# Kernel optimization log

Hardware: AMD Instinct MI355X
Metric: run time of the kernel (lower is better)

## Reference

```python
import jax, jax.numpy as jnp
import numpy as np

S = 3072       # packed sequence length
DIM = 1280     # hidden dim
H = 16         # num heads
HD = DIM // H  # head dim = 80
NEG = -1e9     # additive mask value for cross-segment entries


def setup_inputs() -> dict:
    key = jax.random.key(0)
    ks = jax.random.split(key, 6)
    x = jax.random.normal(ks[0], (S, DIM), jnp.float32)
    # rope angle table [S, HD//2]
    rotary_pos_emb = jax.random.uniform(ks[1], (S, HD // 2), jnp.float32, 0.0, 2.0 * np.pi)
    # 4 equal image segments packed together
    cu_seqlens = jnp.array([0, 768, 1536, 2304, 3072], jnp.int32)
    w_qkv = jax.random.normal(ks[2], (3 * DIM, DIM), jnp.float32) * 0.02
    b_qkv = jax.random.normal(ks[3], (3 * DIM,), jnp.float32) * 0.02
    w_proj = jax.random.normal(ks[4], (DIM, DIM), jnp.float32) * 0.02
    b_proj = jax.random.normal(ks[5], (DIM,), jnp.float32) * 0.02
    return {"x": x, "cu_seqlens": cu_seqlens, "rotary_pos_emb": rotary_pos_emb,
            "w_qkv": w_qkv, "b_qkv": b_qkv, "w_proj": w_proj, "b_proj": b_proj}


def _rope(t, cos, sin):
    # t: [S, H, HD]; cos/sin: [S, 1, HD]
    t1, t2 = jnp.split(t, 2, axis=-1)
    rot = jnp.concatenate([-t2, t1], axis=-1)
    return t * cos + rot * sin


def reference(x, cu_seqlens, rotary_pos_emb, w_qkv, b_qkv, w_proj, b_proj):
    s, d = x.shape
    qkv = (x @ w_qkv.T + b_qkv).reshape(s, 3, H, HD)
    q, k, v = qkv[:, 0], qkv[:, 1], qkv[:, 2]  # each [S, H, HD]

    # NeoX-style rope with tiled (repeated) freqs, computed in fp32
    cos = jnp.cos(rotary_pos_emb)
    sin = jnp.sin(rotary_pos_emb)
    cos = jnp.concatenate([cos, cos], axis=-1)[:, None, :]  # [S,1,HD]
    sin = jnp.concatenate([sin, sin], axis=-1)[:, None, :]
    q = _rope(q.astype(jnp.float32), cos, sin).astype(x.dtype)
    k = _rope(k.astype(jnp.float32), cos, sin).astype(x.dtype)

    # block-diagonal varlen mask from cu_seqlens: segment id per position
    seg = jnp.searchsorted(cu_seqlens, jnp.arange(s), side='right') - 1  # [S]
    mask = jnp.where(seg[:, None] == seg[None, :], 0.0, NEG).astype(x.dtype)  # [S,S]

    scale = 1.0 / np.sqrt(HD).astype(np.float32)
    scores = jnp.einsum('qhd,khd->hqk', q, k) * scale + mask[None]  # [H,S,S]
    attn = jax.nn.softmax(scores, axis=-1)
    out = jnp.einsum('hqk,khd->qhd', attn, v).reshape(s, d)  # [S, DIM]
    return out @ w_proj.T + b_proj
```

## Files before the change

### kernel.cpp

```cpp
#include <hip/hip_runtime.h>


typedef __bf16 bf16;
typedef __bf16 bf16x4 __attribute__((ext_vector_type(4)));
typedef __bf16 bf16x8 __attribute__((ext_vector_type(8)));
typedef float f32x4 __attribute__((ext_vector_type(4)));
typedef float f32x16 __attribute__((ext_vector_type(16)));
typedef unsigned int u32;

constexpr int S = 3072;
constexpr int DIM = 1280;
constexpr int H = 16;
constexpr int HD = 80;
constexpr int KDP = 128;
constexpr int NQKV = 3 * DIM;

constexpr int MB_A = S / 256;
constexpr int NB_B = NQKV / 256;
constexpr int NKT = DIM / 32;

constexpr float QSCALE = 1.4426950408889634f / 8.94427190999916f;

__device__ __forceinline__ void gload_lds16(const void* g, void* l) {
  __builtin_amdgcn_global_load_lds(
      (const __attribute__((address_space(1))) void*)g,
      (__attribute__((address_space(3))) void*)l, 16, 0, 0);
}

__device__ __forceinline__ u32 pkbf2(float a, float b) {
  union { bf16 h[2]; u32 w; } u;
  u.h[0] = (bf16)a; u.h[1] = (bf16)b;
  return u.w;
}

constexpr long PA_CHUNKS = (long)MB_A * NKT * 1024;
constexpr long PB_CHUNKS = (long)NB_B * NKT * 1024;
constexpr long PW_CHUNKS = (long)DIM * DIM / 8;

__global__ __launch_bounds__(256) void pack_inputs(
    const float* __restrict__ x, const float* __restrict__ wq,
    const float* __restrict__ wp, bf16* __restrict__ pA,
    bf16* __restrict__ pB, bf16* __restrict__ wp16) {
  long t = (long)blockIdx.x * 256 + threadIdx.x;
  const float* src;
  bf16* dst;
  if (t < PA_CHUNKS + PB_CHUNKS) {
    int blk, rem;
    const float* base;
    bf16* obase;
    if (t < PA_CHUNKS) {
      blk = (int)(t / (NKT * 1024)); rem = (int)(t % (NKT * 1024));
      base = x; obase = pA + t * 8;
    } else {
      long t2 = t - PA_CHUNKS;
      blk = (int)(t2 / (NKT * 1024)); rem = (int)(t2 % (NKT * 1024));
      base = wq; obase = pB + t2 * 8;
    }
    const int kt = rem >> 10, c = rem & 1023;
    const int lin = c * 16;
    const int logi = lin ^ (((lin >> 7) & 7) << 4);
    const int row = logi >> 6, col = (logi & 63) >> 1;
    src = base + (size_t)(blk * 256 + row) * DIM + kt * 32 + col;
    dst = obase;
  } else {
    long t2 = t - PA_CHUNKS - PB_CHUNKS;
    src = wp + t2 * 8;
    dst = wp16 + t2 * 8;
  }
  float4 v0 = *(const float4*)src;
  float4 v1 = *(const float4*)(src + 4);
  bf16x8 o = {(bf16)v0.x, (bf16)v0.y, (bf16)v0.z, (bf16)v0.w,
              (bf16)v1.x, (bf16)v1.y, (bf16)v1.z, (bf16)v1.w};
  *(bf16x8*)dst = o;
}

template <bool OUT_BF16>
__global__ __launch_bounds__(512, 2) void gemm256(
    const bf16* __restrict__ pA, const bf16* __restrict__ pB,
    const float* __restrict__ bias, void* __restrict__ Cout, int M, int N,
    int K) {
  extern __shared__ char lds[];
  const int tid = threadIdx.x;
  const int w = tid >> 6, lane = tid & 63;
  const int r15 = lane & 15, b4 = lane >> 4;
  const int wr = w >> 2, wc = w & 3;
  const int nwg = gridDim.x * gridDim.y;
  const int orig = blockIdx.y * gridDim.x + blockIdx.x;
  const int xcd = orig % 8, loc = orig / 8;
  const int qq = nwg / 8, rq = nwg % 8;
  const int swzid =
      (xcd < rq ? xcd * (qq + 1) : rq * (qq + 1) + (xcd - rq) * qq) + loc;
  const int nb = swzid % gridDim.x, mb = swzid / gridDim.x;
  const int n0 = nb * 256, m0 = mb * 256;
  const char* aPanel = (const char*)pA + (size_t)mb * NKT * 16384;
  const char* bPanel = (const char*)pB + (size_t)nb * NKT * 16384;
  const int NT = K / 32;
  auto stageA = [&](int kt) {
    char* s = lds + (kt & 3) * 32768;
    const char* g = aPanel + (size_t)kt * 16384;
    gload_lds16(g + tid * 16, s + tid * 16);
    gload_lds16(g + 8192 + tid * 16, s + 8192 + tid * 16);
  };
  auto stageB = [&](int kt) {
    char* s = lds + (kt & 3) * 32768 + 16384;
    const char* g = bPanel + (size_t)kt * 16384;
    gload_lds16(g + tid * 16, s + tid * 16);
    gload_lds16(g + 8192 + tid * 16, s + 8192 + tid * 16);
  };
  f32x4 acc[8][4] = {};
  stageA(0); stageB(0); stageA(1); stageB(1); stageA(2); stageB(2);
  asm volatile("s_waitcnt vmcnt(8)" ::: "memory");
  __builtin_amdgcn_s_barrier();
  for (int kt = 0; kt < NT; ++kt) {
    const char* As = lds + (kt & 3) * 32768;
    const char* Bs = As + 16384;
    const bool pf = (kt + 3 < NT);
    bf16x8 afr[4], bfr[4];
#pragma unroll
    for (int i = 0; i < 4; i++) {
      int a = (wr * 128 + i * 16 + r15) * 64 + b4 * 16;
      a ^= ((a >> 7) & 7) << 4;
      afr[i] = *(const bf16x8*)(As + a);
    }
#pragma unroll
    for (int j = 0; j < 4; j++) {
      int a = (wc * 64 + j * 16 + r15) * 64 + b4 * 16;
      a ^= ((a >> 7) & 7) << 4;
      bfr[j] = *(const bf16x8*)(Bs + a);
    }
    if (pf) stageA(kt + 3);
    asm volatile("" ::: "memory");
    __builtin_amdgcn_s_barrier();
    __builtin_amdgcn_s_setprio(1);
#pragma unroll
    for (int i = 0; i < 4; i++)
#pragma unroll
      for (int j = 0; j < 4; j++)
        acc[i][j] = __builtin_amdgcn_mfma_f32_16x16x32_bf16(afr[i], bfr[j],
                                                            acc[i][j], 0, 0, 0);
    __builtin_amdgcn_s_setprio(0);
    asm volatile("" ::: "memory");
    __builtin_amdgcn_s_barrier();
#pragma unroll
    for (int i = 0; i < 4; i++) {
      int a = (wr * 128 + 64 + i * 16 + r15) * 64 + b4 * 16;
      a ^= ((a >> 7) & 7) << 4;
      afr[i] = *(const bf16x8*)(As + a);
    }
    if (pf) stageB(kt + 3);
    asm volatile("" ::: "memory");
    __builtin_amdgcn_s_barrier();
    __builtin_amdgcn_s_setprio(1);
#pragma unroll
    for (int i = 0; i < 4; i++)
#pragma unroll
      for (int j = 0; j < 4; j++)
        acc[4 + i][j] = __builtin_amdgcn_mfma_f32_16x16x32_bf16(
            afr[i], bfr[j], acc[4 + i][j], 0, 0, 0);
    __builtin_amdgcn_s_setprio(0);
    const int rem = NT - 2 - kt;
    if (rem >= 2)      asm volatile("s_waitcnt vmcnt(8)" ::: "memory");
    else if (rem == 1) asm volatile("s_waitcnt vmcnt(4)" ::: "memory");
    else if (rem == 0) asm volatile("s_waitcnt vmcnt(0)" ::: "memory");
    else               asm volatile("" ::: "memory");
    __builtin_amdgcn_s_barrier();
  }
#pragma unroll
  for (int j = 0; j < 4; j++) {
    const int n = n0 + wc * 64 + j * 16 + r15;
    const float bv = bias[n];
#pragma unroll
    for (int i = 0; i < 8; i++) {
      const int mr = m0 + wr * 128 + i * 16 + b4 * 4;
#pragma unroll
      for (int r = 0; r < 4; r++) {
        float v = acc[i][j][r] + bv;
        if (OUT_BF16)
          ((bf16*)Cout)[(size_t)(mr + r) * N + n] = (bf16)v;
        else
          ((float*)Cout)[(size_t)(mr + r) * N + n] = v;
      }
    }
  }
}

template <bool OUT_BF16>
__global__ __launch_bounds__(256) void gemm_bt(
    const bf16* __restrict__ A, const bf16* __restrict__ B,
    const float* __restrict__ bias, void* __restrict__ Cout, int M, int N,
    int K) {
  __shared__ bf16 Al[2][128 * 32];
  __shared__ bf16 Bl[2][128 * 32];
  const int tid = threadIdx.x;
  const int w = tid >> 6, lane = tid & 63;
  const int r15 = lane & 15, b4 = lane >> 4;
  const int nwg = gridDim.x * gridDim.y;
  const int orig = blockIdx.y * gridDim.x + blockIdx.x;
  const int swzid = (orig & 7) * (nwg >> 3) + (orig >> 3);
  const int bx = swzid % gridDim.x, by = swzid / gridDim.x;
  const int m0 = by * 128, n0 = bx * 128;
  const int wm = (w >> 1) * 64, wn = (w & 1) * 64;
  f32x4 acc[4][4] = {};
  const int row0 = tid >> 2, ko0 = (tid & 3) * 8;
  const bf16* Ar0 = A + (size_t)(m0 + row0) * K + ko0;
  const bf16* Ar1 = A + (size_t)(m0 + row0 + 64) * K + ko0;
  const bf16* Br0 = B + (size_t)(n0 + row0) * K + ko0;
  const bf16* Br1 = B + (size_t)(n0 + row0 + 64) * K + ko0;

  auto stage = [&](int buf, int k0) {
    char* la = (char*)Al[buf] + w * 1024;
    char* lb = (char*)Bl[buf] + w * 1024;
    gload_lds16(Ar0 + k0, la);
    gload_lds16(Ar1 + k0, la + 4096);
    gload_lds16(Br0 + k0, lb);
    gload_lds16(Br1 + k0, lb + 4096);
  };

  stage(0, 0);
  int cur = 0;
  for (int k0 = 0; k0 < K; k0 += 32) {
    __syncthreads();
    if (k0 + 32 < K) stage(cur ^ 1, k0 + 32);
    bf16x8 af[4], bfr[4];
#pragma unroll
    for (int i = 0; i < 4; i++) {
      af[i] = *(const bf16x8*)((const char*)Al[cur] + (wm + i * 16 + r15) * 64 + b4 * 16);
      bfr[i] = *(const bf16x8*)((const char*)Bl[cur] + (wn + i * 16 + r15) * 64 + b4 * 16);
    }
#pragma unroll
    for (int i = 0; i < 4; i++)
#pragma unroll
      for (int j = 0; j < 4; j++)
        acc[i][j] = __builtin_amdgcn_mfma_f32_16x16x32_bf16(af[i], bfr[j], acc[i][j], 0, 0, 0);
    cur ^= 1;
  }
#pragma unroll
  for (int j = 0; j < 4; j++) {
    const int n = n0 + wn + j * 16 + r15;
    const float bv = bias[n];
#pragma unroll
    for (int i = 0; i < 4; i++) {
      const int mr = m0 + wm + i * 16 + b4 * 4;
#pragma unroll
      for (int r = 0; r < 4; r++) {
        float v = acc[i][j][r] + bv;
        if (OUT_BF16)
          ((bf16*)Cout)[(size_t)(mr + r) * N + n] = (bf16)v;
        else
          ((float*)Cout)[(size_t)(mr + r) * N + n] = v;
      }
    }
  }
}

__global__ __launch_bounds__(256) void rope_scatter(
    const bf16* __restrict__ qkv, const float* __restrict__ rp,
    bf16* __restrict__ Qo, bf16* __restrict__ Ko, bf16* __restrict__ VTo) {
  __shared__ bf16 vl[80][72];
  const int h = blockIdx.x / 48, st = blockIdx.x % 48;
  const int tid = threadIdx.x;
#pragma unroll
  for (int c = 0; c < 3; c++) {
    int ch = c * 256 + tid;
    if (ch < 640) {
      int row = ch / 10, ck = ch % 10;
      int s = st * 64 + row;
      bf16x8 v = *(const bf16x8*)(qkv + (size_t)s * NQKV + 2 * DIM + h * HD + ck * 8);
#pragma unroll
      for (int e = 0; e < 8; e++) vl[ck * 8 + e][row] = v[e];
    }
  }
#pragma unroll
  for (int c = 0; c < 3; c++) {
    int ch = c * 256 + tid;
    if (ch < 640) {
      int row = ch / 10, t10 = ch % 10;
      int which = t10 >= 5 ? 1 : 0, cp = t10 % 5;
      int s = st * 64 + row;
      const bf16* src = qkv + (size_t)s * NQKV + which * DIM + h * HD;
      bf16x8 lo = *(const bf16x8*)(src + cp * 8);
      bf16x8 hi = *(const bf16x8*)(src + 40 + cp * 8);
      const float* rr = rp + (size_t)s * 40 + cp * 8;
      float4 a0 = *(const float4*)rr;
      float4 a1 = *(const float4*)(rr + 4);
      float ang[8] = {a0.x, a0.y, a0.z, a0.w, a1.x, a1.y, a1.z, a1.w};
      const float sc = which ? 1.0f : QSCALE;
      bf16x8 olo, ohi;
#pragma unroll
      for (int e = 0; e < 8; e++) {
        float sn, cs;
        __sincosf(ang[e], &sn, &cs);
        float t1 = (float)lo[e], t2 = (float)hi[e];
        olo[e] = (bf16)((t1 * cs - t2 * sn) * sc);
        ohi[e] = (bf16)((t2 * cs + t1 * sn) * sc);
      }
      bf16* dst = which ? (Ko + ((size_t)h * S + s) * KDP)
                        : (Qo + ((size_t)h * S + s) * HD);
      *(bf16x8*)(dst + cp * 8) = olo;
      *(bf16x8*)(dst + 40 + cp * 8) = ohi;
    }
  }
#pragma unroll
  for (int c = 0; c < 2; c++) {
    int ch = c * 256 + tid;
    if (ch < 384) {
      int row = ch / 6, cc = ch % 6;
      bf16x8 z = {};
      *(bf16x8*)(Ko + ((size_t)h * S + st * 64 + row) * KDP + 80 + cc * 8) = z;
    }
  }
  __syncthreads();
#pragma unroll
  for (int c = 0; c < 3; c++) {
    int ch = c * 256 + tid;
    if (ch < 640) {
      int d = ch >> 3, slot = ch & 7;
      *(bf16x8*)(VTo + (size_t)(h * HD + d) * S + st * 64 + slot * 8) =
          *(const bf16x8*)(&vl[d][slot * 8]);
    }
  }
}

__global__ __launch_bounds__(256) void attn_kern(
    const bf16* __restrict__ Qg, const bf16* __restrict__ Kg,
    const bf16* __restrict__ Vg, const int* __restrict__ cu, int nseg,
    bf16* __restrict__ Out) {
  __shared__ bf16 Kl[2][64 * 128];
  __shared__ bf16 Vl[2][96 * 64];
  const int tid = threadIdx.x, w = tid >> 6, lane = tid & 63;
  const int r31 = lane & 31, hi = lane >> 5;
  const int nwg = gridDim.x;
  const int orig = blockIdx.x;
  const int swzb = (orig & 7) * (nwg >> 3) + (orig >> 3);
  const int h = swzb / 24, qb = swzb % 24;
  const int q = qb * 128 + w * 32 + r31;
  int sq = 0, eq = S, lo = 0, hik = S;
  {
    const int qlo = qb * 128, qhi = qb * 128 + 127;
#pragma unroll
    for (int i = 0; i < 8; i++) {
      if (i >= nseg) break;
      int a = cu[i], b = cu[i + 1];
      if (q >= a && q < b) { sq = a; eq = b; }
      if (qlo >= a && qlo < b) lo = a;
      if (qhi >= a && qhi < b) hik = b;
    }
  }
  {
    int b = tid >> 7, o = (tid & 127) * 16;
    bf16x8 z = {};
    *(bf16x8*)((char*)Vl[b] + 10240 + o) = z;
  }
  bf16x8 qf[5];
  {
    const bf16* qrow = Qg + ((size_t)h * S + q) * HD + hi * 8;
#pragma unroll
    for (int kk = 0; kk < 5; kk++) qf[kk] = *(const bf16x8*)(qrow + kk * 16);
  }
  int kdst[4], ksrc[4], vdst[3], vsrc[3];
#pragma unroll
  for (int c = 0; c < 4; c++) {
    int lin = (c * 256 + tid) * 16;
    int row = lin >> 8, colb = (lin & 255) ^ ((row & 15) << 4);
    kdst[c] = lin; ksrc[c] = row * KDP + colb / 2;
  }
#pragma unroll
  for (int c = 0; c < 3; c++) {
    int lin = (c * 256 + tid) * 16;
    int row = lin >> 7, colb = (lin & 127) ^ ((row & 7) << 4);
    vdst[c] = lin; vsrc[c] = row * S + colb / 2;
  }
  const bf16* Kbase = Kg + (size_t)h * S * KDP;
  const bf16* Vbase = Vg + (size_t)h * HD * S;
  auto stage = [&](int buf, int k0) {
#pragma unroll
    for (int c = 0; c < 4; c++)
      gload_lds16(Kbase + (size_t)k0 * KDP + ksrc[c], (char*)Kl[buf] + kdst[c]);
#pragma unroll
    for (int c = 0; c < 3; c++)
      if (c < 2 || tid < 128)
        gload_lds16(Vbase + vsrc[c] + k0, (char*)Vl[buf] + vdst[c]);
  };
  f32x16 o0 = {}, o1 = {}, o2 = {};
  float m = -1e30f, l = 0.f;
  const int k0s = lo & ~63;
  stage(0, k0s);
  asm volatile("s_waitcnt vmcnt(0)" ::: "memory");
  __syncthreads();
  int cur = 0;
  for (int k0 = k0s; k0 < hik; k0 += 64) {
    const bool more = (k0 + 64 < hik);
    if (more) stage(cur ^ 1, k0 + 64);
    f32x16 st0 = {}, st1 = {};
    __builtin_amdgcn_s_setprio(1);
#pragma unroll
    for (int kk = 0; kk < 5; kk++) {
      const int colb = kk * 32 + hi * 16;
      bf16x8 kf0 = *(const bf16x8*)((const char*)Kl[cur] +
                                    r31 * 256 + (colb ^ ((r31 & 15) << 4)));
      bf16x8 kf1 = *(const bf16x8*)((const char*)Kl[cur] + (32 + r31) * 256 +
                                    (colb ^ ((r31 & 15) << 4)));
      st0 = __builtin_amdgcn_mfma_f32_32x32x16_bf16(kf0, qf[kk], st0, 0, 0, 0);
      st1 = __builtin_amdgcn_mfma_f32_32x32x16_bf16(kf1, qf[kk], st1, 0, 0, 0);
    }
    __builtin_amdgcn_s_setprio(0);
    float tm = -3e38f;
    if (k0 >= sq && k0 + 63 < eq) {
#pragma unroll
      for (int j = 0; j < 16; j++) {
        tm = fmaxf(tm, st0[j]);
        tm = fmaxf(tm, st1[j]);
      }
    } else {
#pragma unroll
      for (int j = 0; j < 16; j++) {
        const int crow = (j & 3) + 8 * (j >> 2) + 4 * hi;
        int key0 = k0 + crow, key1 = k0 + 32 + crow;
        st0[j] = (key0 >= sq && key0 < eq) ? st0[j] : -1e30f;
        st1[j] = (key1 >= sq && key1 < eq) ? st1[j] : -1e30f;
        tm = fmaxf(tm, st0[j]);
        tm = fmaxf(tm, st1[j]);
      }
    }
    tm = fmaxf(tm, __shfl_xor(tm, 32));
    if (!__all(tm <= m + 8.f)) {
      const float mn = fmaxf(m, tm);
      const float alpha = __builtin_amdgcn_exp2f(m - mn);
      o0 *= alpha; o1 *= alpha; o2 *= alpha;
      l *= alpha;
      m = mn;
    }
    float rs = 0.f;
    u32 wd0[4][2], wd1[4][2];
#pragma unroll
    for (int g2 = 0; g2 < 4; g2++) {
#pragma unroll
      for (int hh = 0; hh < 2; hh++) {
        float a0 = __builtin_amdgcn_exp2f(st0[g2 * 4 + 2 * hh] - m);
        float a1 = __builtin_amdgcn_exp2f(st0[g2 * 4 + 2 * hh + 1] - m);
        float b0 = __builtin_amdgcn_exp2f(st1[g2 * 4 + 2 * hh] - m);
        float b1 = __builtin_amdgcn_exp2f(st1[g2 * 4 + 2 * hh + 1] - m);
        rs += a0 + a1 + b0 + b1;
        wd0[g2][hh] = pkbf2(a0, a1);
        wd1[g2][hh] = pkbf2(b0, b1);
      }
    }
    rs += __shfl_xor(rs, 32);
    l += rs;
    __builtin_amdgcn_s_setprio(1);
#pragma unroll
    for (int kk = 0; kk < 4; kk++) {
      const int g2o = (kk & 1) * 2 + hi;
      const int g2s = (kk & 1) * 2 + (hi ^ 1);
      u32 own0, own1, snd0, snd1;
      if (kk < 2) {
        own0 = wd0[g2o][0]; own1 = wd0[g2o][1];
        snd0 = wd0[g2s][0]; snd1 = wd0[g2s][1];
      } else {
        own0 = wd1[g2o][0]; own1 = wd1[g2o][1];
        snd0 = wd1[g2s][0]; snd1 = wd1[g2s][1];
      }
      u32 rc0 = (u32)__shfl_xor((int)snd0, 32);
      u32 rc1 = (u32)__shfl_xor((int)snd1, 32);
      union { u32 w[4]; bf16x8 v; } pf;
      if (hi == 0) { pf.w[0] = own0; pf.w[1] = own1; pf.w[2] = rc0; pf.w[3] = rc1; }
      else         { pf.w[0] = rc0;  pf.w[1] = rc1;  pf.w[2] = own0; pf.w[3] = own1; }
      const int colb = kk * 32 + hi * 16;
#pragma unroll
      for (int mt = 0; mt < 3; mt++) {
        const int row = mt * 32 + r31;
        bf16x8 vf = *(const bf16x8*)((const char*)Vl[cur] + row * 128 +
                                     (colb ^ ((row & 7) << 4)));
        f32x16 * op = mt == 0 ? &o0 : (mt == 1 ? &o1 : &o2);
        *op = __builtin_amdgcn_mfma_f32_32x32x16_bf16(vf, pf.v, *op, 0, 0, 0);
      }
    }
    __builtin_amdgcn_s_setprio(0);
    asm volatile("s_waitcnt vmcnt(0)" ::: "memory");
    __syncthreads();
    cur ^= 1;
  }
  const float inv = 1.f / l;
  bf16* orow = Out + (size_t)q * DIM + h * HD;
#pragma unroll
  for (int rg = 0; rg < 4; rg++) {
    bf16x4 v0 = {(bf16)(o0[rg * 4] * inv), (bf16)(o0[rg * 4 + 1] * inv),
                 (bf16)(o0[rg * 4 + 2] * inv), (bf16)(o0[rg * 4 + 3] * inv)};
    *(bf16x4*)(orow + 8 * rg + 4 * hi) = v0;
    bf16x4 v1 = {(bf16)(o1[rg * 4] * inv), (bf16)(o1[rg * 4 + 1] * inv),
                 (bf16)(o1[rg * 4 + 2] * inv), (bf16)(o1[rg * 4 + 3] * inv)};
    *(bf16x4*)(orow + 32 + 8 * rg + 4 * hi) = v1;
  }
#pragma unroll
  for (int rg = 0; rg < 2; rg++) {
    bf16x4 v2 = {(bf16)(o2[rg * 4] * inv), (bf16)(o2[rg * 4 + 1] * inv),
                 (bf16)(o2[rg * 4 + 2] * inv), (bf16)(o2[rg * 4 + 3] * inv)};
    *(bf16x4*)(orow + 64 + 8 * rg + 4 * hi) = v2;
  }
}

extern "C" void kernel_launch(void* const* d_in, const int* in_sizes, int n_in,
                              void* d_out, int out_size, void* d_ws,
                              size_t ws_size, hipStream_t stream) {
  const float* x = (const float*)d_in[0];
  const int* cu = (const int*)d_in[1];
  const float* rope = (const float*)d_in[2];
  const float* w_qkv = (const float*)d_in[3];
  const float* b_qkv = (const float*)d_in[4];
  const float* w_proj = (const float*)d_in[5];
  const float* b_proj = (const float*)d_in[6];
  const int nseg = in_sizes[1] - 1;

  bf16* pA = (bf16*)d_ws;
  bf16* pB = pA + (size_t)S * DIM;
  bf16* wp16 = pB + (size_t)NQKV * DIM;
  bf16* qkv16 = wp16 + (size_t)DIM * DIM;
  bf16* Qb = qkv16 + (size_t)S * NQKV;
  bf16* Kb = Qb + (size_t)H * S * HD;
  bf16* VTb = Kb + (size_t)H * S * KDP;
  bf16* attn16 = pA;

  const long total_chunks = PA_CHUNKS + PB_CHUNKS + PW_CHUNKS;
  pack_inputs<<<(int)(total_chunks / 256), 256, 0, stream>>>(
      x, w_qkv, w_proj, pA, pB, wp16);
  gemm256<true><<<dim3(NQKV / 256, S / 256), 512, 131072, stream>>>(
      pA, pB, b_qkv, qkv16, S, NQKV, DIM);
  rope_scatter<<<H * 48, 256, 0, stream>>>(qkv16, rope, Qb, Kb, VTb);
  attn_kern<<<H * 24, 256, 0, stream>>>(Qb, Kb, VTb, cu, nseg, attn16);
  gemm_bt<false><<<dim3(DIM / 128, S / 128), 256, 0, stream>>>(
      attn16, wp16, b_proj, d_out, S, DIM, DIM);
}
```

Baseline: 132.4 us.

## Fuse RoPE and Q/K/V scatter into the QKV GEMM epilogue

The rope_scatter kernel is removed. The QKV GEMM epilogue now applies the bias, RoPE and Q scaling, and writes Q, K and transposed V directly through an LDS staging buffer. To make this work, the Q/K weight rows are permuted during packing so that each rotary pair sits in adjacent columns and can be exchanged with a lane shuffle. Cos/sin tables and K padding zeroing move into the pack kernel. This removes one launch and the bf16 qkv intermediate round-trip through memory, at the cost of a heavier GEMM epilogue, extra table traffic and LDS reuse with an extra barrier.

New measurement: 131.3 us. About the same (-0.8%).

```diff
diff --git a/kernel.cpp b/kernel.cpp
--- a/kernel.cpp
+++ b/kernel.cpp
@@ -33,21 +33,28 @@
   return u.w;
 }
 
+__device__ __forceinline__ int swv(int s) {
+  return ((((s >> 3) & 31) ^ ((s & 7) << 2)) << 2);
+}
+
 constexpr long PA_CHUNKS = (long)MB_A * NKT * 1024;
 constexpr long PB_CHUNKS = (long)NB_B * NKT * 1024;
 constexpr long PW_CHUNKS = (long)DIM * DIM / 8;
+constexpr long KP_CHUNKS = (long)H * S * 48 / 8;
+constexpr long CS_CHUNKS = (long)S * 40 / 8;
+constexpr long TOT_CHUNKS = PA_CHUNKS + PB_CHUNKS + PW_CHUNKS + KP_CHUNKS + CS_CHUNKS;
 
 __global__ __launch_bounds__(256) void pack_inputs(
     const float* __restrict__ x, const float* __restrict__ wq,
-    const float* __restrict__ wp, bf16* __restrict__ pA,
-    bf16* __restrict__ pB, bf16* __restrict__ wp16) {
+    const float* __restrict__ wp, const float* __restrict__ rope,
+    bf16* __restrict__ pA, bf16* __restrict__ pB, bf16* __restrict__ wp16,
+    bf16* __restrict__ Kb, float* __restrict__ ctab, float* __restrict__ stab) {
   long t = (long)blockIdx.x * 256 + threadIdx.x;
-  const float* src;
-  bf16* dst;
   if (t < PA_CHUNKS + PB_CHUNKS) {
     int blk, rem;
     const float* base;
     bf16* obase;
+    bool isB = false;
     if (t < PA_CHUNKS) {
       blk = (int)(t / (NKT * 1024)); rem = (int)(t % (NKT * 1024));
       base = x; obase = pA + t * 8;
@@ -55,30 +62,58 @@
       long t2 = t - PA_CHUNKS;
       blk = (int)(t2 / (NKT * 1024)); rem = (int)(t2 % (NKT * 1024));
       base = wq; obase = pB + t2 * 8;
+      isB = true;
     }
     const int kt = rem >> 10, c = rem & 1023;
     const int lin = c * 16;
     const int logi = lin ^ (((lin >> 7) & 7) << 4);
-    const int row = logi >> 6, col = (logi & 63) >> 1;
-    src = base + (size_t)(blk * 256 + row) * DIM + kt * 32 + col;
-    dst = obase;
+    int row = logi >> 6;
+    const int col = (logi & 63) >> 1;
+    int grow = blk * 256 + row;
+    if (isB && grow < 2560) {
+      const int ty = grow / 1280, rm = grow % 1280;
+      const int h = rm / 80, p = rm % 80;
+      grow = ty * 1280 + h * 80 + (p >> 1) + (p & 1) * 40;
+    }
+    const float* src = base + (size_t)grow * DIM + kt * 32 + col;
+    float4 v0 = *(const float4*)src;
+    float4 v1 = *(const float4*)(src + 4);
+    bf16x8 o = {(bf16)v0.x, (bf16)v0.y, (bf16)v0.z, (bf16)v0.w,
+                (bf16)v1.x, (bf16)v1.y, (bf16)v1.z, (bf16)v1.w};
+    *(bf16x8*)obase = o;
+  } else if (t < PA_CHUNKS + PB_CHUNKS + PW_CHUNKS) {
+    long t2 = t - PA_CHUNKS - PB_CHUNKS;
+    const float* src = wp + t2 * 8;
+    float4 v0 = *(const float4*)src;
+    float4 v1 = *(const float4*)(src + 4);
+    bf16x8 o = {(bf16)v0.x, (bf16)v0.y, (bf16)v0.z, (bf16)v0.w,
+                (bf16)v1.x, (bf16)v1.y, (bf16)v1.z, (bf16)v1.w};
+    *(bf16x8*)(wp16 + t2 * 8) = o;
+  } else if (t < PA_CHUNKS + PB_CHUNKS + PW_CHUNKS + KP_CHUNKS) {
+    long t2 = t - PA_CHUNKS - PB_CHUNKS - PW_CHUNKS;
+    const int h = (int)(t2 / (S * 6)), r = (int)(t2 % (S * 6));
+    const int s = r / 6, cc = r % 6;
+    bf16x8 z = {};
+    *(bf16x8*)(Kb + ((size_t)h * S + s) * KDP + 80 + cc * 8) = z;
   } else {
-    long t2 = t - PA_CHUNKS - PB_CHUNKS;
-    src = wp + t2 * 8;
-    dst = wp16 + t2 * 8;
-  }
-  float4 v0 = *(const float4*)src;
-  float4 v1 = *(const float4*)(src + 4);
-  bf16x8 o = {(bf16)v0.x, (bf16)v0.y, (bf16)v0.z, (bf16)v0.w,
-              (bf16)v1.x, (bf16)v1.y, (bf16)v1.z, (bf16)v1.w};
-  *(bf16x8*)dst = o;
-}
-
-template <bool OUT_BF16>
+    long t3 = t - PA_CHUNKS - PB_CHUNKS - PW_CHUNKS - KP_CHUNKS;
+#pragma unroll
+    for (int k = 0; k < 8; k++) {
+      const int idx = (int)(t3 * 8 + k);
+      const int s = idx / 40, a = idx % 40;
+      float sn, cs;
+      __sincosf(rope[idx], &sn, &cs);
+      ctab[a * S + s] = cs;
+      stab[a * S + s] = sn;
+    }
+  }
+}
+
 __global__ __launch_bounds__(512, 2) void gemm256(
     const bf16* __restrict__ pA, const bf16* __restrict__ pB,
-    const float* __restrict__ bias, void* __restrict__ Cout, int M, int N,
-    int K) {
+    const float* __restrict__ bias, const float* __restrict__ ctab,
+    const float* __restrict__ stab, bf16* __restrict__ Qb,
+    bf16* __restrict__ Kb, bf16* __restrict__ VTb) {
   extern __shared__ char lds[];
   const int tid = threadIdx.x;
   const int w = tid >> 6, lane = tid & 63;
@@ -91,10 +126,9 @@
   const int swzid =
       (xcd < rq ? xcd * (qq + 1) : rq * (qq + 1) + (xcd - rq) * qq) + loc;
   const int nb = swzid % gridDim.x, mb = swzid / gridDim.x;
-  const int n0 = nb * 256, m0 = mb * 256;
+  const int m0 = mb * 256;
   const char* aPanel = (const char*)pA + (size_t)mb * NKT * 16384;
   const char* bPanel = (const char*)pB + (size_t)nb * NKT * 16384;
-  const int NT = K / 32;
   auto stageA = [&](int kt) {
     char* s = lds + (kt & 3) * 32768;
     const char* g = aPanel + (size_t)kt * 16384;
@@ -111,10 +145,10 @@
   stageA(0); stageB(0); stageA(1); stageB(1); stageA(2); stageB(2);
   asm volatile("s_waitcnt vmcnt(8)" ::: "memory");
   __builtin_amdgcn_s_barrier();
-  for (int kt = 0; kt < NT; ++kt) {
+  for (int kt = 0; kt < NKT; ++kt) {
     const char* As = lds + (kt & 3) * 32768;
     const char* Bs = As + 16384;
-    const bool pf = (kt + 3 < NT);
+    const bool pf = (kt + 3 < NKT);
     bf16x8 afr[4], bfr[4];
 #pragma unroll
     for (int i = 0; i < 4; i++) {
@@ -158,28 +192,79 @@
         acc[4 + i][j] = __builtin_amdgcn_mfma_f32_16x16x32_bf16(
             afr[i], bfr[j], acc[4 + i][j], 0, 0, 0);
     __builtin_amdgcn_s_setprio(0);
-    const int rem = NT - 2 - kt;
+    const int rem = NKT - 2 - kt;
     if (rem >= 2)      asm volatile("s_waitcnt vmcnt(8)" ::: "memory");
     else if (rem == 1) asm volatile("s_waitcnt vmcnt(4)" ::: "memory");
     else if (rem == 0) asm volatile("s_waitcnt vmcnt(0)" ::: "memory");
     else               asm volatile("" ::: "memory");
     __builtin_amdgcn_s_barrier();
   }
-#pragma unroll
-  for (int j = 0; j < 4; j++) {
-    const int n = n0 + wc * 64 + j * 16 + r15;
-    const float bv = bias[n];
-#pragma unroll
-    for (int i = 0; i < 8; i++) {
-      const int mr = m0 + wr * 128 + i * 16 + b4 * 4;
-#pragma unroll
-      for (int r = 0; r < 4; r++) {
-        float v = acc[i][j][r] + bv;
-        if (OUT_BF16)
-          ((bf16*)Cout)[(size_t)(mr + r) * N + n] = (bf16)v;
-        else
-          ((float*)Cout)[(size_t)(mr + r) * N + n] = v;
-      }
+  const int n0 = nb * 256;
+  const int type = n0 / 1280;
+  const int cpart0 = n0 - type * 1280;
+  if (type < 2) {
+#pragma unroll
+    for (int j = 0; j < 4; j++) {
+      const int c = wc * 64 + j * 16 + r15;
+      const int cp = cpart0 + c;
+      const int h = cp / 80, p = cp % 80;
+      const int d = (p >> 1) + (p & 1) * 40;
+      const float bv = bias[type * 1280 + h * 80 + d];
+      const int a = p >> 1;
+#pragma unroll
+      for (int i = 0; i < 8; i++) {
+        const int sl = wr * 128 + i * 16 + b4 * 4;
+        f32x4 cs4 = *(const f32x4*)&ctab[a * S + m0 + sl];
+        f32x4 sn4 = *(const f32x4*)&stab[a * S + m0 + sl];
+#pragma unroll
+        for (int r = 0; r < 4; r++) {
+          float v = acc[i][j][r] + bv;
+          float ov = __shfl_xor(v, 1);
+          float res = (p & 1) ? (v * cs4[r] + ov * sn4[r])
+                              : (v * cs4[r] - ov * sn4[r]);
+          if (type == 0) res *= QSCALE;
+          *(bf16*)(lds + (sl + r) * 512 + ((2 * c) ^ (((sl + r) & 7) << 4))) =
+              (bf16)res;
+        }
+      }
+    }
+    __syncthreads();
+#pragma unroll
+    for (int t = 0; t < 16; t++) {
+      const int task = t * 512 + tid;
+      const int sl = task >> 5, c = (task & 31) * 8;
+      bf16x8 v = *(const bf16x8*)(lds + sl * 512 + ((2 * c) ^ ((sl & 7) << 4)));
+      const int cp = cpart0 + c, h = cp / 80, p = cp % 80;
+      bf16* dst = type ? Kb + ((size_t)h * S + m0 + sl) * KDP + p
+                       : Qb + ((size_t)h * S + m0 + sl) * HD + p;
+      *(bf16x8*)dst = v;
+    }
+  } else {
+#pragma unroll
+    for (int j = 0; j < 4; j++) {
+      const int c = wc * 64 + j * 16 + r15;
+      const float bv = bias[2560 + cpart0 + c];
+#pragma unroll
+      for (int i = 0; i < 8; i++) {
+        const int sl = wr * 128 + i * 16 + b4 * 4;
+#pragma unroll
+        for (int r = 0; r < 4; r++) {
+          *(bf16*)(lds + (sl + r) * 512 + ((2 * c) ^ swv(sl + r))) =
+              (bf16)(acc[i][j][r] + bv);
+        }
+      }
+    }
+    __syncthreads();
+#pragma unroll
+    for (int t = 0; t < 16; t++) {
+      const int task = t * 512 + tid;
+      const int c = task >> 5, s0 = (task & 31) * 8;
+      union { bf16 h[8]; bf16x8 v; } o;
+#pragma unroll
+      for (int e = 0; e < 8; e++)
+        o.h[e] = *(const bf16*)(lds + (s0 + e) * 512 + ((2 * c) ^ swv(s0 + e)));
+      const int cp = cpart0 + c, h = cp / 80, d = cp % 80;
+      *(bf16x8*)(VTb + ((size_t)(h * 80 + d)) * S + m0 + s0) = o.v;
     }
   }
 }
@@ -253,74 +338,6 @@
   }
 }
 
-__global__ __launch_bounds__(256) void rope_scatter(
-    const bf16* __restrict__ qkv, const float* __restrict__ rp,
-    bf16* __restrict__ Qo, bf16* __restrict__ Ko, bf16* __restrict__ VTo) {
-  __shared__ bf16 vl[80][72];
-  const int h = blockIdx.x / 48, st = blockIdx.x % 48;
-  const int tid = threadIdx.x;
-#pragma unroll
-  for (int c = 0; c < 3; c++) {
-    int ch = c * 256 + tid;
-    if (ch < 640) {
-      int row = ch / 10, ck = ch % 10;
-      int s = st * 64 + row;
-      bf16x8 v = *(const bf16x8*)(qkv + (size_t)s * NQKV + 2 * DIM + h * HD + ck * 8);
-#pragma unroll
-      for (int e = 0; e < 8; e++) vl[ck * 8 + e][row] = v[e];
-    }
-  }
-#pragma unroll
-  for (int c = 0; c < 3; c++) {
-    int ch = c * 256 + tid;
-    if (ch < 640) {
-      int row = ch / 10, t10 = ch % 10;
-      int which = t10 >= 5 ? 1 : 0, cp = t10 % 5;
-      int s = st * 64 + row;
-      const bf16* src = qkv + (size_t)s * NQKV + which * DIM + h * HD;
-      bf16x8 lo = *(const bf16x8*)(src + cp * 8);
-      bf16x8 hi = *(const bf16x8*)(src + 40 + cp * 8);
-      const float* rr = rp + (size_t)s * 40 + cp * 8;
-      float4 a0 = *(const float4*)rr;
-      float4 a1 = *(const float4*)(rr + 4);
-      float ang[8] = {a0.x, a0.y, a0.z, a0.w, a1.x, a1.y, a1.z, a1.w};
-      const float sc = which ? 1.0f : QSCALE;
-      bf16x8 olo, ohi;
-#pragma unroll
-      for (int e = 0; e < 8; e++) {
-        float sn, cs;
-        __sincosf(ang[e], &sn, &cs);
-        float t1 = (float)lo[e], t2 = (float)hi[e];
-        olo[e] = (bf16)((t1 * cs - t2 * sn) * sc);
-        ohi[e] = (bf16)((t2 * cs + t1 * sn) * sc);
-      }
-      bf16* dst = which ? (Ko + ((size_t)h * S + s) * KDP)
-                        : (Qo + ((size_t)h * S + s) * HD);
-      *(bf16x8*)(dst + cp * 8) = olo;
-      *(bf16x8*)(dst + 40 + cp * 8) = ohi;
-    }
-  }
-#pragma unroll
-  for (int c = 0; c < 2; c++) {
-    int ch = c * 256 + tid;
-    if (ch < 384) {
-      int row = ch / 6, cc = ch % 6;
-      bf16x8 z = {};
-      *(bf16x8*)(Ko + ((size_t)h * S + st * 64 + row) * KDP + 80 + cc * 8) = z;
-    }
-  }
-  __syncthreads();
-#pragma unroll
-  for (int c = 0; c < 3; c++) {
-    int ch = c * 256 + tid;
-    if (ch < 640) {
-      int d = ch >> 3, slot = ch & 7;
-      *(bf16x8*)(VTo + (size_t)(h * HD + d) * S + st * 64 + slot * 8) =
-          *(const bf16x8*)(&vl[d][slot * 8]);
-    }
-  }
-}
-
 __global__ __launch_bounds__(256) void attn_kern(
     const bf16* __restrict__ Qg, const bf16* __restrict__ Kg,
     const bf16* __restrict__ Vg, const int* __restrict__ cu, int nseg,
@@ -514,18 +531,17 @@
   bf16* pA = (bf16*)d_ws;
   bf16* pB = pA + (size_t)S * DIM;
   bf16* wp16 = pB + (size_t)NQKV * DIM;
-  bf16* qkv16 = wp16 + (size_t)DIM * DIM;
-  bf16* Qb = qkv16 + (size_t)S * NQKV;
+  bf16* Qb = wp16 + (size_t)DIM * DIM;
   bf16* Kb = Qb + (size_t)H * S * HD;
   bf16* VTb = Kb + (size_t)H * S * KDP;
+  float* ctab = (float*)(VTb + (size_t)H * HD * S);
+  float* stab = ctab + (size_t)S * 40;
   bf16* attn16 = pA;
 
-  const long total_chunks = PA_CHUNKS + PB_CHUNKS + PW_CHUNKS;
-  pack_inputs<<<(int)(total_chunks / 256), 256, 0, stream>>>(
-      x, w_qkv, w_proj, pA, pB, wp16);
-  gemm256<true><<<dim3(NQKV / 256, S / 256), 512, 131072, stream>>>(
-      pA, pB, b_qkv, qkv16, S, NQKV, DIM);
-  rope_scatter<<<H * 48, 256, 0, stream>>>(qkv16, rope, Qb, Kb, VTb);
+  pack_inputs<<<(int)(TOT_CHUNKS / 256), 256, 0, stream>>>(
+      x, w_qkv, w_proj, rope, pA, pB, wp16, Kb, ctab, stab);
+  gemm256<<<dim3(NB_B, MB_A), 512, 131072, stream>>>(
+      pA, pB, b_qkv, ctab, stab, Qb, Kb, VTb);
   attn_kern<<<H * 24, 256, 0, stream>>>(Qb, Kb, VTb, cu, nseg, attn16);
   gemm_bt<false><<<dim3(DIM / 128, S / 128), 256, 0, stream>>>(
       attn16, wp16, b_proj, d_out, S, DIM, DIM);
```
